# Kernel tuning notes

Hardware: AMD Instinct MI355X
Metric: run time of the kernel (lower is better)

The kernel has to match this reference:

```python
import jax, jax.numpy as jnp
import numpy as np

N_VERTICES = 50000
N_FEATURES = 128
N_EDGES = 640000


def setup_inputs() -> dict:
    key = jax.random.key(0)
    k1, k2, k3, k4 = jax.random.split(key, 4)
    inp = jax.random.normal(k1, (N_VERTICES, N_FEATURES), dtype=jnp.float32)
    eidx = jax.random.randint(k2, (2, N_EDGES), 0, N_VERTICES, dtype=jnp.int64)
    enorm = jax.random.uniform(k3, (N_EDGES,), dtype=jnp.float32)
    esgn = jnp.sign(jax.random.normal(k4, (N_EDGES,), dtype=jnp.float32))
    return {"input": inp, "eidx": eidx, "enorm": enorm, "esgn": esgn}


def reference(input, eidx, enorm, esgn):
    sidx, tidx = eidx[0], eidx[1]
    # gather source node features, scale by signed normalized edge weight
    message = input[sidx] * (esgn * enorm)[:, None]  # [n_edges, d]
    # scatter-add messages onto target nodes
    res = jax.ops.segment_sum(message, tidx, num_segments=input.shape[0])
    return res
```

## Files before the change

kernel.cpp:

```cpp
#include <hip/hip_runtime.h>
#include <hip/hip_fp16.h>


#define N_V 50000
#define N_F 128
#define N_E 640000
#define CAP 64

#define SCAT_BLKS (N_E / 256)
#define CVT_BLKS  (N_V * N_F / 8 / 256)

typedef float f32x4 __attribute__((ext_vector_type(4)));

__global__ void __launch_bounds__(256) gc_prep(
    const int* __restrict__ sidx, const int* __restrict__ tidx,
    const float* __restrict__ enorm, const float* __restrict__ esgn,
    const float* __restrict__ input,
    int* __restrict__ cnt, unsigned int* __restrict__ bucket,
    __half* __restrict__ tab)
{
    if (blockIdx.x < SCAT_BLKS) {
        const int e = blockIdx.x * 256 + threadIdx.x;
        const int t = tidx[e];
        const int s = sidx[e];
        const float w = esgn[e] * enorm[e];
        const int pos = atomicAdd(&cnt[t], 1);
        if (pos < CAP) {
            const unsigned rec =
                ((unsigned)__half_as_ushort(__float2half_rn(w)) << 16)
                | (unsigned)s;
            bucket[(size_t)t * CAP + pos] = rec;
        }
    } else {
        const size_t i = (size_t)(blockIdx.x - SCAT_BLKS) * 256 + threadIdx.x;
        const size_t base = i * 8;
        const f32x4 a = *reinterpret_cast<const f32x4*>(input + base);
        const f32x4 b = *reinterpret_cast<const f32x4*>(input + base + 4);
        uint4 pk;
        pk.x = (unsigned)__half_as_ushort(__float2half_rn(a.x))
             | ((unsigned)__half_as_ushort(__float2half_rn(a.y)) << 16);
        pk.y = (unsigned)__half_as_ushort(__float2half_rn(a.z))
             | ((unsigned)__half_as_ushort(__float2half_rn(a.w)) << 16);
        pk.z = (unsigned)__half_as_ushort(__float2half_rn(b.x))
             | ((unsigned)__half_as_ushort(__float2half_rn(b.y)) << 16);
        pk.w = (unsigned)__half_as_ushort(__float2half_rn(b.z))
             | ((unsigned)__half_as_ushort(__float2half_rn(b.w)) << 16);
        *reinterpret_cast<uint4*>(tab + base) = pk;
    }
}

__global__ void __launch_bounds__(256) gc_gather_h(
    const __half* __restrict__ tab, const int* __restrict__ cnt,
    const unsigned int* __restrict__ bucket, float* __restrict__ out)
{
    const int v = blockIdx.x * 4 + (threadIdx.x >> 6);
    if (v >= N_V) return;
    const int lane  = threadIdx.x & 63;
    const int half_ = lane >> 5;
    const int q     = (lane & 31) * 4;

    const int n = min(cnt[v], CAP);
    unsigned rec = 0;
    if (lane < n)
        rec = __builtin_nontemporal_load(bucket + (size_t)v * CAP + lane);
    const int   rs = (int)(rec & 0xffffu);
    const float rw = __half2float(__ushort_as_half((unsigned short)(rec >> 16)));

    f32x4 acc = (f32x4)0.f;
    const int nIter = (n + 1) >> 1;
    int k = 0;
    for (; k + 2 <= nIter; k += 2) {
        const int i0 = 2 * k + half_;
        const int i1 = 2 * k + 2 + half_;
        const int   s0 = __shfl(rs, i0);
        const float w0 = __shfl(rw, i0);
        const int   s1 = __shfl(rs, i1);
        const float w1 = __shfl(rw, i1);
        const uint2 u0 = *reinterpret_cast<const uint2*>(tab + (size_t)s0 * N_F + q);
        const uint2 u1 = *reinterpret_cast<const uint2*>(tab + (size_t)s1 * N_F + q);
        const float2 a0 = __half22float2(*reinterpret_cast<const __half2*>(&u0.x));
        const float2 b0 = __half22float2(*reinterpret_cast<const __half2*>(&u0.y));
        const float2 a1 = __half22float2(*reinterpret_cast<const __half2*>(&u1.x));
        const float2 b1 = __half22float2(*reinterpret_cast<const __half2*>(&u1.y));
        acc.x += a0.x * w0; acc.y += a0.y * w0; acc.z += b0.x * w0; acc.w += b0.y * w0;
        acc.x += a1.x * w1; acc.y += a1.y * w1; acc.z += b1.x * w1; acc.w += b1.y * w1;
    }
    if (k < nIter) {
        const int i0 = 2 * k + half_;
        const int   s0 = __shfl(rs, i0);
        const float w0 = __shfl(rw, i0);
        const uint2 u0 = *reinterpret_cast<const uint2*>(tab + (size_t)s0 * N_F + q);
        const float2 a0 = __half22float2(*reinterpret_cast<const __half2*>(&u0.x));
        const float2 b0 = __half22float2(*reinterpret_cast<const __half2*>(&u0.y));
        acc.x += a0.x * w0; acc.y += a0.y * w0; acc.z += b0.x * w0; acc.w += b0.y * w0;
    }

    acc.x += __shfl(acc.x, lane + 32);
    acc.y += __shfl(acc.y, lane + 32);
    acc.z += __shfl(acc.z, lane + 32);
    acc.w += __shfl(acc.w, lane + 32);

    if (half_ == 0) {
        __builtin_nontemporal_store(acc,
            reinterpret_cast<f32x4*>(out + (size_t)v * N_F + q));
    }
}

__global__ void __launch_bounds__(256) gc_atomic_fallback(
    const float* __restrict__ input, const int* __restrict__ sidx,
    const int* __restrict__ tidx, const float* __restrict__ enorm,
    const float* __restrict__ esgn, float* __restrict__ out)
{
    const int e = blockIdx.x * 8 + (threadIdx.x >> 5);
    if (e >= N_E) return;
    const int lane = threadIdx.x & 31;
    const int s = sidx[e], t = tidx[e];
    const float w = esgn[e] * enorm[e];
    float4 v = reinterpret_cast<const float4*>(input + (size_t)s * N_F)[lane];
    float* orow = out + (size_t)t * N_F + lane * 4;
    atomicAdd(orow + 0, v.x * w);
    atomicAdd(orow + 1, v.y * w);
    atomicAdd(orow + 2, v.z * w);
    atomicAdd(orow + 3, v.w * w);
}

extern "C" void kernel_launch(void* const* d_in, const int* in_sizes, int n_in,
                              void* d_out, int out_size, void* d_ws, size_t ws_size,
                              hipStream_t stream) {
    const float* input = (const float*)d_in[0];
    const int*   eidx  = (const int*)d_in[1];
    const float* enorm = (const float*)d_in[2];
    const float* esgn  = (const float*)d_in[3];
    float* out = (float*)d_out;

    const int* sidx = eidx;
    const int* tidx = eidx + N_E;

    const size_t need = (size_t)N_V * sizeof(int)
                      + (size_t)N_V * CAP * sizeof(unsigned int)
                      + (size_t)N_V * N_F * sizeof(__half);

    if (ws_size >= need) {
        int*          cnt    = (int*)d_ws;
        unsigned int* bucket = (unsigned int*)(cnt + N_V);
        __half*       tab    = (__half*)(bucket + (size_t)N_V * CAP);
        hipMemsetAsync(cnt, 0, (size_t)N_V * sizeof(int), stream);
        hipLaunchKernelGGL(gc_prep, dim3(SCAT_BLKS + CVT_BLKS), dim3(256),
                           0, stream, sidx, tidx, enorm, esgn, input,
                           cnt, bucket, tab);
        hipLaunchKernelGGL(gc_gather_h, dim3((N_V + 3) / 4), dim3(256),
                           0, stream, tab, cnt, bucket, out);
    } else {
        hipMemsetAsync(d_out, 0, (size_t)out_size * sizeof(float), stream);
        hipLaunchKernelGGL(gc_atomic_fallback, dim3(N_E / 8), dim3(256), 0,
                           stream, input, sidx, tidx, enorm, esgn, out);
    }
}
```

Measured before the change: 148.9 us.

## Partition edge bucketing by target residue mod 8 with split counter arrays

The scatter phase now launches eight blocks per edge chunk. Each block handles only the edges whose target index falls in its residue class mod 8, and those edges atomically increment a counter in a separate per-residue array. The intent is to keep each block's atomics and bucket writes on a disjoint subset of counters and cache lines (probably aiming for XCD or L2 locality), cutting atomic contention and cross-cache traffic. In exchange, every chunk's tidx is read eight times and seven eighths of the threads exit early, and the gather reads its counters through a strided index.

```diff
diff --git a/kernel.cpp b/kernel.cpp
--- a/kernel.cpp
+++ b/kernel.cpp
@@ -7,8 +7,10 @@
 #define N_E 640000
 #define CAP 64
 
-#define SCAT_BLKS (N_E / 256)
-#define CVT_BLKS  (N_V * N_F / 8 / 256)
+#define SCAT_CHUNKS (N_E / 256)
+#define SCAT_BLKS   (SCAT_CHUNKS * 8)
+#define CVT_BLKS    (N_V * N_F / 8 / 256)
+#define CNT_STRIDE  6272
 
 typedef float f32x4 __attribute__((ext_vector_type(4)));
 
@@ -16,20 +18,24 @@
     const int* __restrict__ sidx, const int* __restrict__ tidx,
     const float* __restrict__ enorm, const float* __restrict__ esgn,
     const float* __restrict__ input,
-    int* __restrict__ cnt, unsigned int* __restrict__ bucket,
+    int* __restrict__ cnt2, unsigned int* __restrict__ bucket,
     __half* __restrict__ tab)
 {
     if (blockIdx.x < SCAT_BLKS) {
-        const int e = blockIdx.x * 256 + threadIdx.x;
+        const int chunk = blockIdx.x >> 3;
+        const int myres = blockIdx.x & 7;
+        const int e = chunk * 256 + threadIdx.x;
         const int t = tidx[e];
-        const int s = sidx[e];
-        const float w = esgn[e] * enorm[e];
-        const int pos = atomicAdd(&cnt[t], 1);
-        if (pos < CAP) {
-            const unsigned rec =
-                ((unsigned)__half_as_ushort(__float2half_rn(w)) << 16)
-                | (unsigned)s;
-            bucket[(size_t)t * CAP + pos] = rec;
+        if ((t & 7) == myres) {
+            const int s = sidx[e];
+            const float w = esgn[e] * enorm[e];
+            const int pos = atomicAdd(&cnt2[myres * CNT_STRIDE + (t >> 3)], 1);
+            if (pos < CAP) {
+                const unsigned rec =
+                    ((unsigned)__half_as_ushort(__float2half_rn(w)) << 16)
+                    | (unsigned)s;
+                bucket[(size_t)t * CAP + pos] = rec;
+            }
         }
     } else {
         const size_t i = (size_t)(blockIdx.x - SCAT_BLKS) * 256 + threadIdx.x;
@@ -50,7 +56,7 @@
 }
 
 __global__ void __launch_bounds__(256) gc_gather_h(
-    const __half* __restrict__ tab, const int* __restrict__ cnt,
+    const __half* __restrict__ tab, const int* __restrict__ cnt2,
     const unsigned int* __restrict__ bucket, float* __restrict__ out)
 {
     const int v = blockIdx.x * 4 + (threadIdx.x >> 6);
@@ -59,7 +65,7 @@
     const int half_ = lane >> 5;
     const int q     = (lane & 31) * 4;
 
-    const int n = min(cnt[v], CAP);
+    const int n = min(cnt2[(v & 7) * CNT_STRIDE + (v >> 3)], CAP);
     unsigned rec = 0;
     if (lane < n)
         rec = __builtin_nontemporal_load(bucket + (size_t)v * CAP + lane);
@@ -136,20 +142,20 @@
     const int* sidx = eidx;
     const int* tidx = eidx + N_E;
 
-    const size_t need = (size_t)N_V * sizeof(int)
+    const size_t need = (size_t)8 * CNT_STRIDE * sizeof(int)
                       + (size_t)N_V * CAP * sizeof(unsigned int)
                       + (size_t)N_V * N_F * sizeof(__half);
 
     if (ws_size >= need) {
-        int*          cnt    = (int*)d_ws;
-        unsigned int* bucket = (unsigned int*)(cnt + N_V);
+        int*          cnt2   = (int*)d_ws;
+        unsigned int* bucket = (unsigned int*)(cnt2 + 8 * CNT_STRIDE);
         __half*       tab    = (__half*)(bucket + (size_t)N_V * CAP);
-        hipMemsetAsync(cnt, 0, (size_t)N_V * sizeof(int), stream);
+        hipMemsetAsync(cnt2, 0, (size_t)8 * CNT_STRIDE * sizeof(int), stream);
         hipLaunchKernelGGL(gc_prep, dim3(SCAT_BLKS + CVT_BLKS), dim3(256),
                            0, stream, sidx, tidx, enorm, esgn, input,
-                           cnt, bucket, tab);
+                           cnt2, bucket, tab);
         hipLaunchKernelGGL(gc_gather_h, dim3((N_V + 3) / 4), dim3(256),
-                           0, stream, tab, cnt, bucket, out);
+                           0, stream, tab, cnt2, bucket, out);
     } else {
         hipMemsetAsync(d_out, 0, (size_t)out_size * sizeof(float), stream);
         hipLaunchKernelGGL(gc_atomic_fallback, dim3(N_E / 8), dim3(256), 0,
```

New measurement: 142.2 us. 1.05x faster.
